# Optimization experiments

Measured on AMD Instinct MI355X. Metric: run time of the kernel, lower is better.

The kernel has to match this reference:

```python
import jax, jax.numpy as jnp
import numpy as np

B, S, D, H = 4, 2048, 1024, 16
HD = D // H  # head_dim = 64

def setup_inputs() -> dict:
    key = jax.random.key(0)
    ks = jax.random.split(key, 5)
    scale = 1.0 / np.sqrt(D)
    return {
        "x": jax.random.normal(ks[0], (B, S, D), dtype=jnp.float32),
        "Wqkv": jax.random.normal(ks[1], (D, 3 * D), dtype=jnp.float32) * scale,
        "bqkv": jax.random.normal(ks[2], (3 * D,), dtype=jnp.float32) * 0.01,
        "Wo": jax.random.normal(ks[3], (D, D), dtype=jnp.float32) * scale,
        "bo": jax.random.normal(ks[4], (D,), dtype=jnp.float32) * 0.01,
    }

def reference(x, Wqkv, bqkv, Wo, bo):
    b, s, d = x.shape
    # fused QKV projection: [B,S,3D]
    qkv = jnp.einsum("bsd,de->bse", x, Wqkv) + bqkv
    # [B,S,H,3*HD] -> [B,H,S,3*HD], then chunk into q,k,v per head
    qkv = qkv.reshape(b, s, H, 3 * HD).transpose(0, 2, 1, 3)
    q, k, v = jnp.split(qkv, 3, axis=-1)  # each [B,H,S,HD]
    inv_sqrt_dk = jnp.asarray(1.0 / np.sqrt(HD), dtype=x.dtype)
    scores = jnp.einsum("bhqd,bhkd->bhqk", q, k) * inv_sqrt_dk
    attn = jax.nn.softmax(scores, axis=-1)
    values = jnp.einsum("bhqk,bhkd->bhqd", attn, v)  # [B,H,S,HD]
    # NOTE: source reshapes [B,H,S,HD] -> [B,S,H*HD] WITHOUT permuting back
    # (a quirk of the original code); replicated faithfully.
    values = values.reshape(b, s, d)
    out = jnp.einsum("bsd,de->bse", values, Wo) + bo
    return out
```

## Files before the change

kernel.cpp:

```cpp
#include <hip/hip_runtime.h>
#include <hip/hip_bf16.h>
#include <cstdint>

static constexpr int Bq  = 4;
static constexpr int Sq  = 2048;
static constexpr int Dq  = 1024;
static constexpr int Hq  = 16;
static constexpr int HDq = 64;
static constexpr int ROWS = Bq * Sq;
static constexpr int QKV_N = 3 * Dq;

typedef __bf16 bf16x8 __attribute__((ext_vector_type(8)));
typedef __bf16 bf16x4 __attribute__((ext_vector_type(4)));
typedef __bf16 bf16x2 __attribute__((ext_vector_type(2)));
typedef float  floatx4 __attribute__((ext_vector_type(4)));
typedef float  floatx16 __attribute__((ext_vector_type(16)));
typedef unsigned int uintx4 __attribute__((ext_vector_type(4)));

#define MFMA16(a, b, c) __builtin_amdgcn_mfma_f32_16x16x32_bf16((a), (b), (c), 0, 0, 0)
#define MFMA32(a, b, c) __builtin_amdgcn_mfma_f32_32x32x16_bf16((a), (b), (c), 0, 0, 0)

#define QSCALE 0.18033688011112042f

__device__ __forceinline__ void async16(const void* g, void* l) {
    __builtin_amdgcn_global_load_lds(
        (const __attribute__((address_space(1))) uint32_t*)g,
        (__attribute__((address_space(3))) uint32_t*)l, 16, 0, 0);
}

__global__ __launch_bounds__(256) void cvt4_kernel(const float4* __restrict__ in,
                                                   bf16x4* __restrict__ out, int n4) {
    int i = blockIdx.x * 256 + threadIdx.x;
    if (i < n4) {
        float4 v = in[i];
        bf16x4 o;
        o[0] = (__bf16)v.x; o[1] = (__bf16)v.y; o[2] = (__bf16)v.z; o[3] = (__bf16)v.w;
        out[i] = o;
    }
}

__global__ __launch_bounds__(256) void tcvt_kernel(const float* __restrict__ in,
                                                   __bf16* __restrict__ out, int K, int N) {
    __shared__ float t[32][33];
    int n0 = blockIdx.x * 32, k0 = blockIdx.y * 32;
    int c = threadIdx.x & 31, r0 = threadIdx.x >> 5;
#pragma unroll
    for (int rr = 0; rr < 32; rr += 8)
        t[r0 + rr][c] = in[(size_t)(k0 + r0 + rr) * N + n0 + c];
    __syncthreads();
#pragma unroll
    for (int rr = 0; rr < 32; rr += 8)
        out[(size_t)(n0 + r0 + rr) * K + k0 + c] = (__bf16)t[c][r0 + rr];
}

template <int MODE>
__global__ __launch_bounds__(256) void gemm_bt_kernel(const __bf16* __restrict__ A,
                                                      const __bf16* __restrict__ BT,
                                                      const float* __restrict__ bias,
                                                      void* __restrict__ Cout,
                                                      __bf16* __restrict__ Vt,
                                                      int M, int N, int K) {
    __shared__ __bf16 As[128 * 32];
    __shared__ __bf16 Bs[128 * 32];

    const int t = threadIdx.x;
    const int lane = t & 63;
    const int wave = t >> 6;
    const int wm = wave & 1, wn = wave >> 1;
    const int l15 = lane & 15;
    const int kg = (lane >> 4) * 8;

    const int m0 = blockIdx.y * 128;
    const int n0 = blockIdx.x * 128;

    const int srow = t >> 2;
    const int scol = (t & 3) * 8;
    const __bf16* ag = A  + (size_t)(m0 + srow) * K + scol;
    const __bf16* bg = BT + (size_t)(n0 + srow) * K + scol;
    __bf16* al = As + t * 8;
    __bf16* bl = Bs + t * 8;

    floatx4 acc[4][4] = {};

    for (int k0 = 0; k0 < K; k0 += 32) {
        __syncthreads();
        async16(ag + k0,                    al);
        async16(ag + (size_t)64 * K + k0,   al + 2048);
        async16(bg + k0,                    bl);
        async16(bg + (size_t)64 * K + k0,   bl + 2048);
        __syncthreads();

        bf16x8 af[4], bfr[4];
#pragma unroll
        for (int mi = 0; mi < 4; ++mi)
            af[mi] = *(const bf16x8*)(As + (wm * 64 + mi * 16 + l15) * 32 + kg);
#pragma unroll
        for (int ni = 0; ni < 4; ++ni)
            bfr[ni] = *(const bf16x8*)(Bs + (wn * 64 + ni * 16 + l15) * 32 + kg);
#pragma unroll
        for (int mi = 0; mi < 4; ++mi)
#pragma unroll
            for (int ni = 0; ni < 4; ++ni)
                acc[mi][ni] = MFMA16(af[mi], bfr[ni], acc[mi][ni]);
    }

    const int r0 = (lane >> 4) * 4;
    const int wn0 = n0 + wn * 64;

    if (MODE == 2 && (wn0 % 192) == 128) {
#pragma unroll
        for (int ni = 0; ni < 4; ++ni) {
            int col = wn0 + ni * 16 + l15;
            float bv = bias[col];
            int h = col / 192;
            int d = col - h * 192 - 128;
#pragma unroll
            for (int mi = 0; mi < 4; ++mi) {
                int row = m0 + wm * 64 + mi * 16 + r0;
                int b = row >> 11, s = row & 2047;
                bf16x4 vv;
#pragma unroll
                for (int i = 0; i < 4; ++i) vv[i] = (__bf16)(acc[mi][ni][i] + bv);
                *(bf16x4*)(Vt + ((size_t)(b * Hq + h) * HDq + d) * Sq + s) = vv;
            }
        }
    } else {
        const float sc = (MODE == 2 && (wn0 % 192) == 0) ? QSCALE : 1.0f;
#pragma unroll
        for (int ni = 0; ni < 4; ++ni) {
            int col = wn0 + ni * 16 + l15;
            float bv = bias[col];
#pragma unroll
            for (int mi = 0; mi < 4; ++mi) {
#pragma unroll
                for (int i = 0; i < 4; ++i) {
                    int row = m0 + wm * 64 + mi * 16 + r0 + i;
                    float v = (acc[mi][ni][i] + bv) * sc;
                    size_t off = (size_t)row * N + col;
                    if (MODE == 1) ((float*)Cout)[off] = v;
                    else           ((__bf16*)Cout)[off] = (__bf16)v;
                }
            }
        }
    }
}

__global__ __launch_bounds__(256, 4) void attn_kernel(const __bf16* __restrict__ qkv,
                                                      const __bf16* __restrict__ Vt,
                                                      __bf16* __restrict__ v2) {
    const int bh = blockIdx.x;
    const int b = bh >> 4, h = bh & 15;
    const int q0 = blockIdx.y * 128;
    const int tid  = threadIdx.x;
    const int lane = tid & 63;
    const int wave = tid >> 6;
    const int l31  = lane & 31;
    const int hi   = lane >> 5;
    const int kx   = l31 & 7;
    const size_t rs = QKV_N;
    const __bf16* base  = qkv + (size_t)b * Sq * rs + (size_t)h * (3 * HDq);
    const __bf16* vbase = Vt + (size_t)bh * HDq * Sq;

    __shared__ alignas(16) __bf16 Ks[2][64][64];
    __shared__ alignas(16) __bf16 Vs[2][64][64];

    bf16x8 qb[4];
    {
        const __bf16* qr = base + (size_t)(q0 + wave * 32 + l31) * rs + hi * 8;
#pragma unroll
        for (int st = 0; st < 4; ++st) qb[st] = *(const bf16x8*)(qr + st * 16);
    }

    const int rA = wave * 8 + (lane >> 3);
    const int rB = rA + 32;
    const int sw = ((lane & 7) ^ (rA & 7)) * 8;
    const __bf16* gK0 = base + HDq + (size_t)rA * rs + sw;
    const __bf16* gK1 = base + HDq + (size_t)rB * rs + sw;
    const __bf16* gV0 = vbase + (size_t)rA * Sq + sw;
    const __bf16* gV1 = vbase + (size_t)rB * Sq + sw;
    const int loff0 = wave * 512 + lane * 8;
    const int loff1 = (4 + wave) * 512 + lane * 8;

    auto STAGE = [&](int bufi, int kt) {
        const size_t ko = (size_t)kt * rs;
        async16(gK0 + ko, &Ks[bufi][0][0] + loff0);
        async16(gK1 + ko, &Ks[bufi][0][0] + loff1);
        async16(gV0 + kt, &Vs[bufi][0][0] + loff0);
        async16(gV1 + kt, &Vs[bufi][0][0] + loff1);
    };

    floatx16 o0 = {}, o1 = {};
    float l_acc = 0.f;

    STAGE(0, 0);
    __syncthreads();

    int cur = 0;
    for (int kt = 0; kt < Sq; kt += 64, cur ^= 1) {
        if (kt + 64 < Sq) STAGE(cur ^ 1, kt + 64);

#pragma unroll
        for (int half = 0; half < 2; ++half) {
            const int key = half * 32 + l31;

            floatx16 c = {};
#pragma unroll
            for (int st = 0; st < 4; ++st) {
                bf16x8 a = *(const bf16x8*)(&Ks[cur][key][((st * 2 + hi) ^ kx) * 8]);
                c = MFMA32(a, qb[st], c);
            }

            unsigned int W[8];
#pragma unroll
            for (int m = 0; m < 8; ++m) {
                float e0 = __builtin_amdgcn_exp2f(c[2 * m]);
                float e1 = __builtin_amdgcn_exp2f(c[2 * m + 1]);
                l_acc += e0 + e1;
                union { bf16x2 v; unsigned int u; } pk;
                pk.v[0] = (__bf16)e0; pk.v[1] = (__bf16)e1;
                W[m] = pk.u;
            }

#pragma unroll
            for (int ks = 0; ks < 2; ++ks) {
                auto r0 = __builtin_amdgcn_permlane32_swap(W[ks * 4 + 0], W[ks * 4 + 2], false, false);
                auto r1 = __builtin_amdgcn_permlane32_swap(W[ks * 4 + 1], W[ks * 4 + 3], false, false);
                uintx4 bb; bb[0] = r0[0]; bb[1] = r1[0]; bb[2] = r0[1]; bb[3] = r1[1];
                bf16x8 pb = __builtin_bit_cast(bf16x8, bb);

                const int kslot = half * 4 + ks * 2 + hi;
                bf16x8 va0 = *(const bf16x8*)(&Vs[cur][l31][(kslot ^ kx) * 8]);
                bf16x8 va1 = *(const bf16x8*)(&Vs[cur][32 + l31][(kslot ^ kx) * 8]);
                o0 = MFMA32(va0, pb, o0);
                o1 = MFMA32(va1, pb, o1);
            }
        }
        __syncthreads();
    }

    float l = l_acc + __shfl_xor(l_acc, 32);
    float rinv = 1.0f / l;

    const int q = q0 + wave * 32 + l31;
    size_t row = (size_t)b * Sq + h * 128 + (q >> 4);
    __bf16* vrow = v2 + row * Dq + (size_t)(q & 15) * 64;
#pragma unroll
    for (int gg = 0; gg < 4; ++gg) {
        bf16x4 ov;
#pragma unroll
        for (int i = 0; i < 4; ++i) ov[i] = (__bf16)(o0[gg * 4 + i] * rinv);
        *(bf16x4*)(vrow + gg * 8 + hi * 4) = ov;
#pragma unroll
        for (int i = 0; i < 4; ++i) ov[i] = (__bf16)(o1[gg * 4 + i] * rinv);
        *(bf16x4*)(vrow + 32 + gg * 8 + hi * 4) = ov;
    }
}

extern "C" void kernel_launch(void* const* d_in, const int* in_sizes, int n_in,
                              void* d_out, int out_size, void* d_ws, size_t ws_size,
                              hipStream_t stream) {
    const float* x    = (const float*)d_in[0];
    const float* Wqkv = (const float*)d_in[1];
    const float* bqkv = (const float*)d_in[2];
    const float* Wo   = (const float*)d_in[3];
    const float* bo   = (const float*)d_in[4];
    float* out = (float*)d_out;

    __bf16* xb    = (__bf16*)d_ws;
    __bf16* WqkvT = xb    + (size_t)ROWS * Dq;
    __bf16* WoT   = WqkvT + (size_t)QKV_N * Dq;
    __bf16* qkvb  = WoT   + (size_t)Dq * Dq;
    __bf16* Vt    = qkvb  + (size_t)ROWS * QKV_N;
    __bf16* v2    = xb;

    const int nx4 = ROWS * Dq / 4;
    cvt4_kernel<<<(nx4 + 255) / 256, 256, 0, stream>>>((const float4*)x, (bf16x4*)xb, nx4);
    tcvt_kernel<<<dim3(QKV_N / 32, Dq / 32), 256, 0, stream>>>(Wqkv, WqkvT, Dq, QKV_N);
    tcvt_kernel<<<dim3(Dq / 32, Dq / 32), 256, 0, stream>>>(Wo, WoT, Dq, Dq);

    gemm_bt_kernel<2><<<dim3(QKV_N / 128, ROWS / 128), 256, 0, stream>>>(
        xb, WqkvT, bqkv, (void*)qkvb, Vt, ROWS, QKV_N, Dq);

    attn_kernel<<<dim3(Bq * Hq, Sq / 128), 256, 0, stream>>>(qkvb, Vt, v2);

    gemm_bt_kernel<1><<<dim3(Dq / 128, ROWS / 128), 256, 0, stream>>>(
        v2, WoT, bo, (void*)out, nullptr, ROWS, Dq, Dq);
}
```

Measured before the change: 292.2 us.

## Process two query groups per wave in attention to reuse K/V tiles

Each attention block now covers 256 queries instead of 128, with each wave handling two 32-query groups that share every K and V fragment loaded from LDS. This halves the number of blocks and the number of times global K/V tiles are staged per query, cutting LDS reads and global traffic per unit of work. In exchange it roughly doubles accumulator and Q register use, lowers launch_bounds occupancy from 4 to 2 blocks per CU, and leaves a smaller grid of 512 blocks.

```diff
diff --git a/kernel.cpp b/kernel.cpp
--- a/kernel.cpp
+++ b/kernel.cpp
@@ -145,12 +145,12 @@
     }
 }
 
-__global__ __launch_bounds__(256, 4) void attn_kernel(const __bf16* __restrict__ qkv,
+__global__ __launch_bounds__(256, 2) void attn_kernel(const __bf16* __restrict__ qkv,
                                                       const __bf16* __restrict__ Vt,
                                                       __bf16* __restrict__ v2) {
     const int bh = blockIdx.x;
     const int b = bh >> 4, h = bh & 15;
-    const int q0 = blockIdx.y * 128;
+    const int q0 = blockIdx.y * 256;
     const int tid  = threadIdx.x;
     const int lane = tid & 63;
     const int wave = tid >> 6;
@@ -164,11 +164,12 @@
     __shared__ alignas(16) __bf16 Ks[2][64][64];
     __shared__ alignas(16) __bf16 Vs[2][64][64];
 
-    bf16x8 qb[4];
-    {
-        const __bf16* qr = base + (size_t)(q0 + wave * 32 + l31) * rs + hi * 8;
-#pragma unroll
-        for (int st = 0; st < 4; ++st) qb[st] = *(const bf16x8*)(qr + st * 16);
+    bf16x8 qb[2][4];
+#pragma unroll
+    for (int qg = 0; qg < 2; ++qg) {
+        const __bf16* qr = base + (size_t)(q0 + wave * 64 + qg * 32 + l31) * rs + hi * 8;
+#pragma unroll
+        for (int st = 0; st < 4; ++st) qb[qg][st] = *(const bf16x8*)(qr + st * 16);
     }
 
     const int rA = wave * 8 + (lane >> 3);
@@ -189,8 +190,30 @@
         async16(gV1 + kt, &Vs[bufi][0][0] + loff1);
     };
 
-    floatx16 o0 = {}, o1 = {};
-    float l_acc = 0.f;
+    auto softmax_pb = [&](const floatx16& c, float& la, bf16x8* pb) {
+        unsigned int W[8];
+        float s0 = 0.f, s1 = 0.f;
+#pragma unroll
+        for (int m = 0; m < 8; ++m) {
+            float e0 = __builtin_amdgcn_exp2f(c[2 * m]);
+            float e1 = __builtin_amdgcn_exp2f(c[2 * m + 1]);
+            s0 += e0; s1 += e1;
+            union { bf16x2 v; unsigned int u; } pk;
+            pk.v[0] = (__bf16)e0; pk.v[1] = (__bf16)e1;
+            W[m] = pk.u;
+        }
+        la += s0 + s1;
+#pragma unroll
+        for (int ks = 0; ks < 2; ++ks) {
+            auto r0 = __builtin_amdgcn_permlane32_swap(W[ks * 4 + 0], W[ks * 4 + 2], false, false);
+            auto r1 = __builtin_amdgcn_permlane32_swap(W[ks * 4 + 1], W[ks * 4 + 3], false, false);
+            uintx4 bb; bb[0] = r0[0]; bb[1] = r1[0]; bb[2] = r0[1]; bb[3] = r1[1];
+            pb[ks] = __builtin_bit_cast(bf16x8, bb);
+        }
+    };
+
+    floatx16 o[2][2] = {};
+    float la0 = 0.f, la1 = 0.f;
 
     STAGE(0, 0);
     __syncthreads();
@@ -203,56 +226,50 @@
         for (int half = 0; half < 2; ++half) {
             const int key = half * 32 + l31;
 
-            floatx16 c = {};
+            floatx16 c0 = {}, c1 = {};
 #pragma unroll
             for (int st = 0; st < 4; ++st) {
                 bf16x8 a = *(const bf16x8*)(&Ks[cur][key][((st * 2 + hi) ^ kx) * 8]);
-                c = MFMA32(a, qb[st], c);
+                c0 = MFMA32(a, qb[0][st], c0);
+                c1 = MFMA32(a, qb[1][st], c1);
             }
 
-            unsigned int W[8];
-#pragma unroll
-            for (int m = 0; m < 8; ++m) {
-                float e0 = __builtin_amdgcn_exp2f(c[2 * m]);
-                float e1 = __builtin_amdgcn_exp2f(c[2 * m + 1]);
-                l_acc += e0 + e1;
-                union { bf16x2 v; unsigned int u; } pk;
-                pk.v[0] = (__bf16)e0; pk.v[1] = (__bf16)e1;
-                W[m] = pk.u;
-            }
+            bf16x8 pb0[2], pb1[2];
+            softmax_pb(c0, la0, pb0);
+            softmax_pb(c1, la1, pb1);
 
 #pragma unroll
             for (int ks = 0; ks < 2; ++ks) {
-                auto r0 = __builtin_amdgcn_permlane32_swap(W[ks * 4 + 0], W[ks * 4 + 2], false, false);
-                auto r1 = __builtin_amdgcn_permlane32_swap(W[ks * 4 + 1], W[ks * 4 + 3], false, false);
-                uintx4 bb; bb[0] = r0[0]; bb[1] = r1[0]; bb[2] = r0[1]; bb[3] = r1[1];
-                bf16x8 pb = __builtin_bit_cast(bf16x8, bb);
-
                 const int kslot = half * 4 + ks * 2 + hi;
                 bf16x8 va0 = *(const bf16x8*)(&Vs[cur][l31][(kslot ^ kx) * 8]);
                 bf16x8 va1 = *(const bf16x8*)(&Vs[cur][32 + l31][(kslot ^ kx) * 8]);
-                o0 = MFMA32(va0, pb, o0);
-                o1 = MFMA32(va1, pb, o1);
+                o[0][0] = MFMA32(va0, pb0[ks], o[0][0]);
+                o[0][1] = MFMA32(va1, pb0[ks], o[0][1]);
+                o[1][0] = MFMA32(va0, pb1[ks], o[1][0]);
+                o[1][1] = MFMA32(va1, pb1[ks], o[1][1]);
             }
         }
         __syncthreads();
     }
 
-    float l = l_acc + __shfl_xor(l_acc, 32);
-    float rinv = 1.0f / l;
-
-    const int q = q0 + wave * 32 + l31;
-    size_t row = (size_t)b * Sq + h * 128 + (q >> 4);
-    __bf16* vrow = v2 + row * Dq + (size_t)(q & 15) * 64;
-#pragma unroll
-    for (int gg = 0; gg < 4; ++gg) {
-        bf16x4 ov;
-#pragma unroll
-        for (int i = 0; i < 4; ++i) ov[i] = (__bf16)(o0[gg * 4 + i] * rinv);
-        *(bf16x4*)(vrow + gg * 8 + hi * 4) = ov;
-#pragma unroll
-        for (int i = 0; i < 4; ++i) ov[i] = (__bf16)(o1[gg * 4 + i] * rinv);
-        *(bf16x4*)(vrow + 32 + gg * 8 + hi * 4) = ov;
+#pragma unroll
+    for (int qg = 0; qg < 2; ++qg) {
+        float lsum = qg ? la1 : la0;
+        float l = lsum + __shfl_xor(lsum, 32);
+        float rinv = 1.0f / l;
+        const int q = q0 + wave * 64 + qg * 32 + l31;
+        size_t row = (size_t)b * Sq + h * 128 + (q >> 4);
+        __bf16* vrow = v2 + row * Dq + (size_t)(q & 15) * 64;
+#pragma unroll
+        for (int gg = 0; gg < 4; ++gg) {
+            bf16x4 ov;
+#pragma unroll
+            for (int i = 0; i < 4; ++i) ov[i] = (__bf16)(o[qg][0][gg * 4 + i] * rinv);
+            *(bf16x4*)(vrow + gg * 8 + hi * 4) = ov;
+#pragma unroll
+            for (int i = 0; i < 4; ++i) ov[i] = (__bf16)(o[qg][1][gg * 4 + i] * rinv);
+            *(bf16x4*)(vrow + 32 + gg * 8 + hi * 4) = ov;
+        }
     }
 }
 
@@ -281,7 +298,7 @@
     gemm_bt_kernel<2><<<dim3(QKV_N / 128, ROWS / 128), 256, 0, stream>>>(
         xb, WqkvT, bqkv, (void*)qkvb, Vt, ROWS, QKV_N, Dq);
 
-    attn_kernel<<<dim3(Bq * Hq, Sq / 128), 256, 0, stream>>>(qkvb, Vt, v2);
+    attn_kernel<<<dim3(Bq * Hq, Sq / 256), 256, 0, stream>>>(qkvb, Vt, v2);
 
     gemm_bt_kernel<1><<<dim3(Dq / 128, ROWS / 128), 256, 0, stream>>>(
         v2, WoT, bo, (void*)out, nullptr, ROWS, Dq, Dq);
```

New measurement: 278.6 us. 4.6% less time.
